# Kernel tuning notes

Measured on AMD Instinct MI355X. Metric: run time of the kernel, lower is better.

The kernel has to match this reference:

```python
import jax, jax.numpy as jnp
import numpy as np

DEPTH = 8
LEAVES = 2 ** DEPTH            # 256 leaf values
N_NODES = 2 ** DEPTH - 1       # 255 internal split nodes
TEMP = 1.0
EPS_P = 1e-5
EPS_V = 1e-10
EPS_MASK = 1e-12


def setup_inputs() -> dict:
    key = jax.random.key(0)
    k1, k2, k3 = jax.random.split(key, 3)
    B, D, O = 8192, 512, 64
    x = jax.random.normal(k1, (B, D), dtype=jnp.float32)
    # BaseSplitter assumed: single linear layer + temperature sigmoid
    Ws = jax.random.normal(k2, (D, N_NODES), dtype=jnp.float32) * (1.0 / np.sqrt(D))
    bs = jnp.zeros((N_NODES,), dtype=jnp.float32)
    # xavier_uniform_ init for leaf value table (LEAVES, O)
    limit = float(np.sqrt(6.0 / (LEAVES + O)))
    value = jax.random.uniform(k3, (LEAVES, O), dtype=jnp.float32, minval=-limit, maxval=limit)
    return {"x": x, "Ws": Ws, "bs": bs, "value": value}


def _sdt_forward(x, Ws, bs, value):
    B = x.shape[0]
    leaves = value.shape[0]
    # splitter: per-node routing probabilities, shape (B, 2^depth - 1)
    probs = jax.nn.sigmoid((x @ Ws + bs) / TEMP)

    accum = jnp.zeros((B, leaves), dtype=jnp.float32)
    reg = jnp.float32(0.0)
    for d in range(DEPTH):  # small fixed loop over tree depth
        s, e = 2 ** d - 1, 2 ** (d + 1) - 1
        p = probs[:, s:e]                     # (B, 2^d) nodes at depth d
        logp = jnp.log(jnp.clip(p, EPS_P))
        log1mp = jnp.log(jnp.clip(1.0 - p, EPS_P))
        # regularization: sum over nodes of mean over batch
        reg = reg + (-0.5) * (2.0 ** (-d)) * jnp.log(jnp.clip(p * (1.0 - p), EPS_P)).mean(axis=0).sum()
        # interleave [logp_i, log1mp_i] per node, then broadcast each entry
        # over its span of leaves/2^(d+1) leaf slots
        contrib = jnp.stack([logp, log1mp], axis=-1).reshape(B, 2 ** (d + 1))
        rep = leaves // (2 ** (d + 1))
        accum = accum + jnp.broadcast_to(contrib[:, :, None], (B, 2 ** (d + 1), rep)).reshape(B, leaves)

    sign = jnp.sign(value)                                    # (L, O)
    logval = jnp.log(jnp.clip(jnp.abs(value), EPS_V))          # (L, O)
    ret = logval[None, :, :] + accum[:, :, None]               # (B, L, O)
    log_pos = jax.nn.logsumexp(ret + jnp.log((sign > 0).astype(jnp.float32) + EPS_MASK), axis=1)
    log_neg = jax.nn.logsumexp(ret + jnp.log((sign < 0).astype(jnp.float32) + EPS_MASK), axis=1)
    out = jnp.exp(log_pos) - jnp.exp(log_neg)                  # (B, O)
    return out, reg


def reference(x, Ws, bs, value):
    return _sdt_forward(x, Ws, bs, value)
```

## Files before the change

kernel.cpp:

```cpp
#include <hip/hip_runtime.h>


typedef __attribute__((ext_vector_type(8))) short short8;
typedef __attribute__((ext_vector_type(4))) float floatx4;

constexpr int O = 64;
constexpr int XSTR = 520;
constexpr int PSTR = 280;
constexpr int LSTR = 260;

__device__ __forceinline__ short f2bf(float f) {
  unsigned u = __builtin_bit_cast(unsigned, f);
  u += 0x7fffu + ((u >> 16) & 1u);
  return (short)(u >> 16);
}
__device__ __forceinline__ float bf2f(short h) {
  unsigned u = ((unsigned)(unsigned short)h) << 16;
  return __builtin_bit_cast(float, u);
}
__device__ __forceinline__ int pk2(short a, short b) {
  return (int)((unsigned short)a | ((unsigned)(unsigned short)b << 16));
}

__global__ __launch_bounds__(256) void sdt_pre(
    const float* __restrict__ Ws, const float* __restrict__ value,
    short* __restrict__ wth, short* __restrict__ wtl,
    short* __restrict__ vt, float* __restrict__ reg_slot)
{
  __shared__ short Th[32 * 72], Tl[32 * 72];
  const int bid = blockIdx.x, t = threadIdx.x;
  if (bid < 64) {
    const int k0 = (bid >> 3) * 64, n0 = (bid & 7) * 32;
    const int nn = t & 31, kk8 = t >> 5;
    const int ng = n0 + nn;
#pragma unroll
    for (int i = 0; i < 8; ++i) {
      const int kk = kk8 + i * 8;
      float f = (ng < 255) ? Ws[(size_t)(k0 + kk) * 255 + ng] : 0.f;
      short h = f2bf(f);
      Th[nn * 72 + kk] = h;
      Tl[nn * 72 + kk] = f2bf(f - bf2f(h));
    }
    __syncthreads();
    const int n2 = t >> 3, kg = (t & 7) * 8;
    short8 h8 = *(const short8*)&Th[n2 * 72 + kg];
    short8 l8 = *(const short8*)&Tl[n2 * 72 + kg];
    *(short8*)&wth[(size_t)(n0 + n2) * 512 + k0 + kg] = h8;
    *(short8*)&wtl[(size_t)(n0 + n2) * 512 + k0 + kg] = l8;
  } else {
    const int e0 = (bid - 64) * 4096 + t;
#pragma unroll
    for (int j = 0; j < 16; ++j) {
      const int e = e0 + j * 256;
      vt[e] = f2bf(value[(e & 255) * O + (e >> 8)]);
    }
    if (bid == 64 && t == 0) *reg_slot = 0.f;
  }
}

__global__ __launch_bounds__(512, 2) void sdt_main(
    const float* __restrict__ x, const short* __restrict__ wth,
    const short* __restrict__ wtl, const short* __restrict__ vt,
    const float* __restrict__ bs, float* __restrict__ out,
    float* __restrict__ reg_out)
{
  __shared__ __align__(16) char smem[32 * XSTR * 2 * 2];
  short* xh_s = (short*)smem;
  short* xl_s = xh_s + 32 * XSTR;
  float* L_s  = (float*)smem;
  short* P_bf = (short*)(smem + 32 * LSTR * 4);
  __shared__ float red_s[8];

  const int t = threadIdx.x, lane = t & 63, w = t >> 6;
  const int q = lane >> 4, r16 = lane & 15;
  const int R0 = blockIdx.x * 32;

  {
    const int row = t >> 4, l4 = (t & 15) * 4;
    const float* xrow = x + (size_t)(R0 + row) * 512;
#pragma unroll
    for (int i = 0; i < 8; ++i) {
      const int k = l4 + i * 64;
      float4 v = *(const float4*)(xrow + k);
      short h0 = f2bf(v.x), h1 = f2bf(v.y), h2 = f2bf(v.z), h3 = f2bf(v.w);
      short g0 = f2bf(v.x - bf2f(h0)), g1 = f2bf(v.y - bf2f(h1));
      short g2 = f2bf(v.z - bf2f(h2)), g3 = f2bf(v.w - bf2f(h3));
      int2 hp; hp.x = pk2(h0, h1); hp.y = pk2(h2, h3);
      int2 lp; lp.x = pk2(g0, g1); lp.y = pk2(g2, g3);
      *(int2*)&xh_s[row * XSTR + k] = hp;
      *(int2*)&xl_s[row * XSTR + k] = lp;
    }
  }
  __syncthreads();

  const short* pwh0 = wth + (size_t)(w * 32 + r16) * 512 + q * 8;
  const short* pwl0 = wtl + (size_t)(w * 32 + r16) * 512 + q * 8;
  const short* pwh1 = pwh0 + 16 * 512;
  const short* pwl1 = pwl0 + 16 * 512;
  const int aoff0 = r16 * XSTR + q * 8;
  const int aoff1 = (16 + r16) * XSTR + q * 8;

  floatx4 acc00 = {0,0,0,0}, acc01 = {0,0,0,0}, acc10 = {0,0,0,0}, acc11 = {0,0,0,0};

  short8 Bh0 = *(const short8*)(pwh0), Bl0 = *(const short8*)(pwl0);
  short8 Bh1 = *(const short8*)(pwh1), Bl1 = *(const short8*)(pwl1);

#pragma unroll
  for (int c = 0; c < 16; ++c) {
    short8 nh0, nl0, nh1, nl1;
    if (c < 15) {
      const int o = (c + 1) * 32;
      nh0 = *(const short8*)(pwh0 + o); nl0 = *(const short8*)(pwl0 + o);
      nh1 = *(const short8*)(pwh1 + o); nl1 = *(const short8*)(pwl1 + o);
    }
    short8 ah0 = *(const short8*)&xh_s[aoff0 + c * 32];
    short8 al0 = *(const short8*)&xl_s[aoff0 + c * 32];
    short8 ah1 = *(const short8*)&xh_s[aoff1 + c * 32];
    short8 al1 = *(const short8*)&xl_s[aoff1 + c * 32];

    acc00 = __builtin_amdgcn_mfma_f32_16x16x32_bf16(ah0, Bh0, acc00, 0, 0, 0);
    acc01 = __builtin_amdgcn_mfma_f32_16x16x32_bf16(ah0, Bh1, acc01, 0, 0, 0);
    acc10 = __builtin_amdgcn_mfma_f32_16x16x32_bf16(ah1, Bh0, acc10, 0, 0, 0);
    acc11 = __builtin_amdgcn_mfma_f32_16x16x32_bf16(ah1, Bh1, acc11, 0, 0, 0);
    acc00 = __builtin_amdgcn_mfma_f32_16x16x32_bf16(ah0, Bl0, acc00, 0, 0, 0);
    acc01 = __builtin_amdgcn_mfma_f32_16x16x32_bf16(ah0, Bl1, acc01, 0, 0, 0);
    acc10 = __builtin_amdgcn_mfma_f32_16x16x32_bf16(ah1, Bl0, acc10, 0, 0, 0);
    acc11 = __builtin_amdgcn_mfma_f32_16x16x32_bf16(ah1, Bl1, acc11, 0, 0, 0);
    acc00 = __builtin_amdgcn_mfma_f32_16x16x32_bf16(al0, Bh0, acc00, 0, 0, 0);
    acc01 = __builtin_amdgcn_mfma_f32_16x16x32_bf16(al0, Bh1, acc01, 0, 0, 0);
    acc10 = __builtin_amdgcn_mfma_f32_16x16x32_bf16(al1, Bh0, acc10, 0, 0, 0);
    acc11 = __builtin_amdgcn_mfma_f32_16x16x32_bf16(al1, Bh1, acc11, 0, 0, 0);

    if (c < 15) { Bh0 = nh0; Bl0 = nl0; Bh1 = nh1; Bl1 = nl1; }
  }
  __syncthreads();

  {
    const int c0 = w * 32 + r16, c1 = c0 + 16;
#pragma unroll
    for (int r = 0; r < 4; ++r) {
      int row0 = q * 4 + r, row1 = row0 + 16;
      L_s[row0 * LSTR + c0] = acc00[r];
      L_s[row0 * LSTR + c1] = acc01[r];
      L_s[row1 * LSTR + c0] = acc10[r];
      L_s[row1 * LSTR + c1] = acc11[r];
    }
  }
  __syncthreads();

  {
    const int col = t & 255, half = t >> 8;
    float rsum = 0.f;
    if (col < 255) {
      float b = bs[col];
      for (int r = half * 16; r < half * 16 + 16; ++r) {
        float z = L_s[r * LSTR + col] + b;
        float p = 1.f / (1.f + __expf(-z));
        L_s[r * LSTR + col] = p;
        rsum += __logf(fmaxf(p * (1.f - p), 1e-5f));
      }
      int dd = 31 - __clz(col + 1);
      rsum *= -0.5f / (8192.0f * (float)(1 << dd));
    }
#pragma unroll
    for (int off = 32; off; off >>= 1) rsum += __shfl_down(rsum, off, 64);
    if (lane == 0) red_s[w] = rsum;
  }
  __syncthreads();
  if (t == 0) {
    float s = 0.f;
#pragma unroll
    for (int i = 0; i < 8; ++i) s += red_s[i];
    atomicAdd(reg_out, s);
  }

  {
    const int g8 = t & 31, rp = t >> 5;
    const int Lb = g8 * 8;
#pragma unroll
    for (int rr = 0; rr < 2; ++rr) {
      const int row = rp * 2 + rr;
      const float* Lr = &L_s[row * LSTR];
      float pre = 1.f;
#pragma unroll
      for (int dd = 0; dd < 5; ++dd) {
        float p = Lr[(1 << dd) - 1 + (Lb >> (8 - dd))];
        float br = ((Lb >> (7 - dd)) & 1) ? (1.f - p) : p;
        pre *= fmaxf(br, 1e-5f);
      }
      float p5 = Lr[31 + g8];
      float s5a = fmaxf(p5, 1e-5f), s5b = fmaxf(1.f - p5, 1e-5f);
      float p6a = Lr[63 + 2 * g8], p6b = Lr[63 + 2 * g8 + 1];
      float p7v[4];
#pragma unroll
      for (int m = 0; m < 4; ++m) p7v[m] = Lr[127 + 4 * g8 + m];
      short8 ph;
#pragma unroll
      for (int j = 0; j < 8; ++j) {
        float s5 = (j & 4) ? s5b : s5a;
        float p6 = (j & 4) ? p6b : p6a;
        float s6 = fmaxf((j & 2) ? (1.f - p6) : p6, 1e-5f);
        float p7 = p7v[j >> 1];
        float s7 = fmaxf((j & 1) ? (1.f - p7) : p7, 1e-5f);
        ph[j] = f2bf(pre * s5 * s6 * s7);
      }
      *(short8*)&P_bf[row * PSTR + Lb] = ph;
    }
  }
  __syncthreads();

  {
    const int tm = w & 1, tn = w >> 1;
    floatx4 C = {0, 0, 0, 0};
    const short* vb = vt + (size_t)(tn * 16 + r16) * 256 + q * 8;
    const short* pa = &P_bf[(tm * 16 + r16) * PSTR + q * 8];
#pragma unroll
    for (int kc = 0; kc < 8; ++kc) {
      short8 A8 = *(const short8*)(pa + kc * 32);
      short8 B8 = *(const short8*)(vb + kc * 32);
      C = __builtin_amdgcn_mfma_f32_16x16x32_bf16(A8, B8, C, 0, 0, 0);
    }
    const int col = tn * 16 + r16;
#pragma unroll
    for (int r = 0; r < 4; ++r) {
      int row = tm * 16 + q * 4 + r;
      out[(size_t)(R0 + row) * O + col] = C[r];
    }
  }
}

extern "C" void kernel_launch(void* const* d_in, const int* in_sizes, int n_in,
                              void* d_out, int out_size, void* d_ws, size_t ws_size,
                              hipStream_t stream) {
  const float* x     = (const float*)d_in[0];
  const float* Ws    = (const float*)d_in[1];
  const float* bs    = (const float*)d_in[2];
  const float* value = (const float*)d_in[3];
  float* outp = (float*)d_out;
  float* reg_slot = outp + (size_t)8192 * O;
  short* wth = (short*)d_ws;
  short* wtl = wth + 256 * 512;
  short* vt  = wtl + 256 * 512;

  sdt_pre<<<68, 256, 0, stream>>>(Ws, value, wth, wtl, vt, reg_slot);
  sdt_main<<<256, 512, 0, stream>>>(x, wth, wtl, vt, bs, outp, reg_slot);
}
```

Measured before the change: 97.15 us.

## Replace split-bf16 three-pass GEMM with single-pass fp16 MFMA and fragment-ordered weights

Switches the router GEMM from a three-term bf16 hi/lo split (three MFMAs per tile) to a single fp16 MFMA pass, and uses fp16 for the leaf-probability/value GEMM too. The preprocessing kernel now writes weights and values in an MFMA-fragment order, so each lane does contiguous 16-byte loads. This removes two thirds of the GEMM MFMA work, half the x staging in LDS and the hi/lo conversion arithmetic. It gives up accuracy: fp16 has fewer mantissa bits than the split scheme, and small leaf probabilities below the fp16 subnormal range may flush.

```diff
diff --git a/kernel.cpp b/kernel.cpp
--- a/kernel.cpp
+++ b/kernel.cpp
@@ -1,7 +1,8 @@
 #include <hip/hip_runtime.h>
 
 
-typedef __attribute__((ext_vector_type(8))) short short8;
+typedef __attribute__((ext_vector_type(8))) _Float16 half8;
+typedef __attribute__((ext_vector_type(4))) _Float16 half4;
 typedef __attribute__((ext_vector_type(4))) float floatx4;
 
 constexpr int O = 64;
@@ -9,66 +10,47 @@
 constexpr int PSTR = 280;
 constexpr int LSTR = 260;
 
-__device__ __forceinline__ short f2bf(float f) {
-  unsigned u = __builtin_bit_cast(unsigned, f);
-  u += 0x7fffu + ((u >> 16) & 1u);
-  return (short)(u >> 16);
-}
-__device__ __forceinline__ float bf2f(short h) {
-  unsigned u = ((unsigned)(unsigned short)h) << 16;
-  return __builtin_bit_cast(float, u);
-}
-__device__ __forceinline__ int pk2(short a, short b) {
-  return (int)((unsigned short)a | ((unsigned)(unsigned short)b << 16));
-}
-
 __global__ __launch_bounds__(256) void sdt_pre(
     const float* __restrict__ Ws, const float* __restrict__ value,
-    short* __restrict__ wth, short* __restrict__ wtl,
-    short* __restrict__ vt, float* __restrict__ reg_slot)
+    _Float16* __restrict__ wt, _Float16* __restrict__ vt,
+    float* __restrict__ reg_slot)
 {
-  __shared__ short Th[32 * 72], Tl[32 * 72];
   const int bid = blockIdx.x, t = threadIdx.x;
   if (bid < 64) {
-    const int k0 = (bid >> 3) * 64, n0 = (bid & 7) * 32;
-    const int nn = t & 31, kk8 = t >> 5;
-    const int ng = n0 + nn;
-#pragma unroll
-    for (int i = 0; i < 8; ++i) {
-      const int kk = kk8 + i * 8;
-      float f = (ng < 255) ? Ws[(size_t)(k0 + kk) * 255 + ng] : 0.f;
-      short h = f2bf(f);
-      Th[nn * 72 + kk] = h;
-      Tl[nn * 72 + kk] = f2bf(f - bf2f(h));
-    }
-    __syncthreads();
-    const int n2 = t >> 3, kg = (t & 7) * 8;
-    short8 h8 = *(const short8*)&Th[n2 * 72 + kg];
-    short8 l8 = *(const short8*)&Tl[n2 * 72 + kg];
-    *(short8*)&wth[(size_t)(n0 + n2) * 512 + k0 + kg] = h8;
-    *(short8*)&wtl[(size_t)(n0 + n2) * 512 + k0 + kg] = l8;
+    const int k0 = bid * 8;
+    const int n = t;
+    const int T = n >> 4, r = n & 15;
+    const int c = k0 >> 5, q = (k0 >> 3) & 3;
+    _Float16 v8[8];
+#pragma unroll
+    for (int kk = 0; kk < 8; ++kk) {
+      float f = (n < 255) ? Ws[(size_t)(k0 + kk) * 255 + n] : 0.f;
+      v8[kk] = (_Float16)f;
+    }
+    *(half8*)&wt[(size_t)(T * 16 + c) * 512 + (q * 16 + r) * 8] = *(half8*)v8;
   } else {
-    const int e0 = (bid - 64) * 4096 + t;
+    const int k0 = (bid - 64) * 64;
 #pragma unroll
     for (int j = 0; j < 16; ++j) {
-      const int e = e0 + j * 256;
-      vt[e] = f2bf(value[(e & 255) * O + (e >> 8)]);
+      int e = t + j * 256;
+      int k = k0 + (e >> 6), n = e & 63;
+      float f = value[(size_t)k * O + n];
+      int T = n >> 4, r = n & 15, kc = k >> 5, q = (k >> 3) & 3, jj = k & 7;
+      vt[(size_t)(T * 8 + kc) * 512 + (q * 16 + r) * 8 + jj] = (_Float16)f;
     }
     if (bid == 64 && t == 0) *reg_slot = 0.f;
   }
 }
 
 __global__ __launch_bounds__(512, 2) void sdt_main(
-    const float* __restrict__ x, const short* __restrict__ wth,
-    const short* __restrict__ wtl, const short* __restrict__ vt,
-    const float* __restrict__ bs, float* __restrict__ out,
-    float* __restrict__ reg_out)
+    const float* __restrict__ x, const _Float16* __restrict__ wt,
+    const _Float16* __restrict__ vt, const float* __restrict__ bs,
+    float* __restrict__ out, float* __restrict__ reg_out)
 {
-  __shared__ __align__(16) char smem[32 * XSTR * 2 * 2];
-  short* xh_s = (short*)smem;
-  short* xl_s = xh_s + 32 * XSTR;
-  float* L_s  = (float*)smem;
-  short* P_bf = (short*)(smem + 32 * LSTR * 4);
+  __shared__ __align__(16) char smem[33280 + 17920];
+  _Float16* xh_s = (_Float16*)smem;
+  float*    L_s  = (float*)smem;
+  _Float16* P_h  = (_Float16*)(smem + 33280);
   __shared__ float red_s[8];
 
   const int t = threadIdx.x, lane = t & 63, w = t >> 6;
@@ -82,56 +64,33 @@
     for (int i = 0; i < 8; ++i) {
       const int k = l4 + i * 64;
       float4 v = *(const float4*)(xrow + k);
-      short h0 = f2bf(v.x), h1 = f2bf(v.y), h2 = f2bf(v.z), h3 = f2bf(v.w);
-      short g0 = f2bf(v.x - bf2f(h0)), g1 = f2bf(v.y - bf2f(h1));
-      short g2 = f2bf(v.z - bf2f(h2)), g3 = f2bf(v.w - bf2f(h3));
-      int2 hp; hp.x = pk2(h0, h1); hp.y = pk2(h2, h3);
-      int2 lp; lp.x = pk2(g0, g1); lp.y = pk2(g2, g3);
-      *(int2*)&xh_s[row * XSTR + k] = hp;
-      *(int2*)&xl_s[row * XSTR + k] = lp;
-    }
-  }
-  __syncthreads();
-
-  const short* pwh0 = wth + (size_t)(w * 32 + r16) * 512 + q * 8;
-  const short* pwl0 = wtl + (size_t)(w * 32 + r16) * 512 + q * 8;
-  const short* pwh1 = pwh0 + 16 * 512;
-  const short* pwl1 = pwl0 + 16 * 512;
-  const int aoff0 = r16 * XSTR + q * 8;
-  const int aoff1 = (16 + r16) * XSTR + q * 8;
+      half4 h = {(_Float16)v.x, (_Float16)v.y, (_Float16)v.z, (_Float16)v.w};
+      *(half4*)&xh_s[row * XSTR + k] = h;
+    }
+  }
+  __syncthreads();
+
+  const _Float16* pb0 = wt + (size_t)(2 * w) * 16 * 512 + lane * 8;
+  const _Float16* pb1 = wt + (size_t)(2 * w + 1) * 16 * 512 + lane * 8;
+  const int a0off = r16 * XSTR, a1off = (16 + r16) * XSTR;
 
   floatx4 acc00 = {0,0,0,0}, acc01 = {0,0,0,0}, acc10 = {0,0,0,0}, acc11 = {0,0,0,0};
-
-  short8 Bh0 = *(const short8*)(pwh0), Bl0 = *(const short8*)(pwl0);
-  short8 Bh1 = *(const short8*)(pwh1), Bl1 = *(const short8*)(pwl1);
+  half8 B0 = *(const half8*)pb0, B1 = *(const half8*)pb1;
 
 #pragma unroll
   for (int c = 0; c < 16; ++c) {
-    short8 nh0, nl0, nh1, nl1;
+    half8 n0, n1;
     if (c < 15) {
-      const int o = (c + 1) * 32;
-      nh0 = *(const short8*)(pwh0 + o); nl0 = *(const short8*)(pwl0 + o);
-      nh1 = *(const short8*)(pwh1 + o); nl1 = *(const short8*)(pwl1 + o);
-    }
-    short8 ah0 = *(const short8*)&xh_s[aoff0 + c * 32];
-    short8 al0 = *(const short8*)&xl_s[aoff0 + c * 32];
-    short8 ah1 = *(const short8*)&xh_s[aoff1 + c * 32];
-    short8 al1 = *(const short8*)&xl_s[aoff1 + c * 32];
-
-    acc00 = __builtin_amdgcn_mfma_f32_16x16x32_bf16(ah0, Bh0, acc00, 0, 0, 0);
-    acc01 = __builtin_amdgcn_mfma_f32_16x16x32_bf16(ah0, Bh1, acc01, 0, 0, 0);
-    acc10 = __builtin_amdgcn_mfma_f32_16x16x32_bf16(ah1, Bh0, acc10, 0, 0, 0);
-    acc11 = __builtin_amdgcn_mfma_f32_16x16x32_bf16(ah1, Bh1, acc11, 0, 0, 0);
-    acc00 = __builtin_amdgcn_mfma_f32_16x16x32_bf16(ah0, Bl0, acc00, 0, 0, 0);
-    acc01 = __builtin_amdgcn_mfma_f32_16x16x32_bf16(ah0, Bl1, acc01, 0, 0, 0);
-    acc10 = __builtin_amdgcn_mfma_f32_16x16x32_bf16(ah1, Bl0, acc10, 0, 0, 0);
-    acc11 = __builtin_amdgcn_mfma_f32_16x16x32_bf16(ah1, Bl1, acc11, 0, 0, 0);
-    acc00 = __builtin_amdgcn_mfma_f32_16x16x32_bf16(al0, Bh0, acc00, 0, 0, 0);
-    acc01 = __builtin_amdgcn_mfma_f32_16x16x32_bf16(al0, Bh1, acc01, 0, 0, 0);
-    acc10 = __builtin_amdgcn_mfma_f32_16x16x32_bf16(al1, Bh0, acc10, 0, 0, 0);
-    acc11 = __builtin_amdgcn_mfma_f32_16x16x32_bf16(al1, Bh1, acc11, 0, 0, 0);
-
-    if (c < 15) { Bh0 = nh0; Bl0 = nl0; Bh1 = nh1; Bl1 = nl1; }
+      n0 = *(const half8*)(pb0 + (c + 1) * 512);
+      n1 = *(const half8*)(pb1 + (c + 1) * 512);
+    }
+    half8 a0 = *(const half8*)&xh_s[a0off + c * 32 + q * 8];
+    half8 a1 = *(const half8*)&xh_s[a1off + c * 32 + q * 8];
+    acc00 = __builtin_amdgcn_mfma_f32_16x16x32_f16(a0, B0, acc00, 0, 0, 0);
+    acc01 = __builtin_amdgcn_mfma_f32_16x16x32_f16(a0, B1, acc01, 0, 0, 0);
+    acc10 = __builtin_amdgcn_mfma_f32_16x16x32_f16(a1, B0, acc10, 0, 0, 0);
+    acc11 = __builtin_amdgcn_mfma_f32_16x16x32_f16(a1, B1, acc11, 0, 0, 0);
+    if (c < 15) { B0 = n0; B1 = n1; }
   }
   __syncthreads();
 
@@ -194,7 +153,7 @@
       float p7v[4];
 #pragma unroll
       for (int m = 0; m < 4; ++m) p7v[m] = Lr[127 + 4 * g8 + m];
-      short8 ph;
+      _Float16 ph[8];
 #pragma unroll
       for (int j = 0; j < 8; ++j) {
         float s5 = (j & 4) ? s5b : s5a;
@@ -202,9 +161,9 @@
         float s6 = fmaxf((j & 2) ? (1.f - p6) : p6, 1e-5f);
         float p7 = p7v[j >> 1];
         float s7 = fmaxf((j & 1) ? (1.f - p7) : p7, 1e-5f);
-        ph[j] = f2bf(pre * s5 * s6 * s7);
+        ph[j] = (_Float16)(pre * s5 * s6 * s7);
       }
-      *(short8*)&P_bf[row * PSTR + Lb] = ph;
+      *(half8*)&P_h[row * PSTR + Lb] = *(half8*)ph;
     }
   }
   __syncthreads();
@@ -212,13 +171,13 @@
   {
     const int tm = w & 1, tn = w >> 1;
     floatx4 C = {0, 0, 0, 0};
-    const short* vb = vt + (size_t)(tn * 16 + r16) * 256 + q * 8;
-    const short* pa = &P_bf[(tm * 16 + r16) * PSTR + q * 8];
+    const _Float16* vb = vt + (size_t)(tn * 8) * 512 + lane * 8;
+    const _Float16* pa = &P_h[(tm * 16 + r16) * PSTR + q * 8];
 #pragma unroll
     for (int kc = 0; kc < 8; ++kc) {
-      short8 A8 = *(const short8*)(pa + kc * 32);
-      short8 B8 = *(const short8*)(vb + kc * 32);
-      C = __builtin_amdgcn_mfma_f32_16x16x32_bf16(A8, B8, C, 0, 0, 0);
+      half8 A8 = *(const half8*)(pa + kc * 32);
+      half8 B8 = *(const half8*)(vb + kc * 512);
+      C = __builtin_amdgcn_mfma_f32_16x16x32_f16(A8, B8, C, 0, 0, 0);
     }
     const int col = tn * 16 + r16;
 #pragma unroll
@@ -238,10 +197,9 @@
   const float* value = (const float*)d_in[3];
   float* outp = (float*)d_out;
   float* reg_slot = outp + (size_t)8192 * O;
-  short* wth = (short*)d_ws;
-  short* wtl = wth + 256 * 512;
-  short* vt  = wtl + 256 * 512;
-
-  sdt_pre<<<68, 256, 0, stream>>>(Ws, value, wth, wtl, vt, reg_slot);
-  sdt_main<<<256, 512, 0, stream>>>(x, wth, wtl, vt, bs, outp, reg_slot);
+  _Float16* wt = (_Float16*)d_ws;
+  _Float16* vt = wt + 256 * 512;
+
+  sdt_pre<<<68, 256, 0, stream>>>(Ws, value, wt, vt, reg_slot);
+  sdt_main<<<256, 512, 0, stream>>>(x, wt, vt, bs, outp, reg_slot);
 }
```

Measured after the change: 84.35 us. 13.2% less time.
